# Kernel optimization log

Hardware: AMD Instinct MI355X
Metric: run time of the kernel (lower is better)

Reference implementation:

```python
import jax, jax.numpy as jnp
import numpy as np

B, D, H, R, OUT = 16384, 1024, 4, 1024, 10
LN_EPS = 1e-5


def setup_inputs() -> dict:
    key = jax.random.key(0)
    ks = jax.random.split(key, 20)
    s_in = 1.0 / np.sqrt(D)
    s_hid = 1.0 / np.sqrt(H * R)
    inp = {
        'x': jax.random.normal(ks[0], (B, D), dtype=jnp.float32),
        # block 1
        'wr1': jax.random.normal(ks[1], (H, R, D), dtype=jnp.float32) * s_in,
        'br1': jnp.zeros((H, R), dtype=jnp.float32),
        'wl1': jax.random.normal(ks[2], (H, R, D), dtype=jnp.float32) * s_in,
        'bl1': jnp.zeros((H, R), dtype=jnp.float32),
        'we1': jax.random.normal(ks[3], (D, H * R), dtype=jnp.float32) * s_hid,
        'be1': jnp.zeros((D,), dtype=jnp.float32),
        'g1': jnp.ones((D,), dtype=jnp.float32),
        'b1': jnp.zeros((D,), dtype=jnp.float32),
        # block 2
        'wr2': jax.random.normal(ks[4], (H, R, D), dtype=jnp.float32) * s_in,
        'br2': jnp.zeros((H, R), dtype=jnp.float32),
        'wl2': jax.random.normal(ks[5], (H, R, D), dtype=jnp.float32) * s_in,
        'bl2': jnp.zeros((H, R), dtype=jnp.float32),
        'we2': jax.random.normal(ks[6], (D, H * R), dtype=jnp.float32) * s_hid,
        'be2': jnp.zeros((D,), dtype=jnp.float32),
        'g2': jnp.ones((D,), dtype=jnp.float32),
        'b2': jnp.zeros((D,), dtype=jnp.float32),
        # final linear
        'wf': jax.random.normal(ks[7], (OUT, D), dtype=jnp.float32) * s_in,
        'bf': jnp.zeros((OUT,), dtype=jnp.float32),
    }
    return inp


def _bilinear_block(x, wr, br, wl, bl, we, be):
    # per-basis right/left projections batched into one einsum each: [B,D] x [H,R,D] -> [B,H,R]
    right = jnp.einsum('bd,hrd->bhr', x, wr) + br
    left = jnp.einsum('bd,hrd->bhr', x, wl) + bl
    # elementwise bilinear interaction, concat bases along last dim -> [B, H*R]
    inter = (right * left).reshape(x.shape[0], -1)
    return inter @ we.T + be  # [B, D_out]


def _layernorm(x, g, b):
    mu = jnp.mean(x, axis=-1, keepdims=True)
    var = jnp.mean(jnp.square(x - mu), axis=-1, keepdims=True)
    return (x - mu) * jax.lax.rsqrt(var + LN_EPS) * g + b


def reference(x, wr1, br1, wl1, bl1, we1, be1, g1, b1,
              wr2, br2, wl2, bl2, we2, be2, g2, b2, wf, bf):
    # block 1: bilinear + residual + layernorm
    h = _layernorm(x + _bilinear_block(x, wr1, br1, wl1, bl1, we1, be1), g1, b1)
    # block 2
    h = _layernorm(h + _bilinear_block(h, wr2, br2, wl2, bl2, we2, be2), g2, b2)
    # final linear head
    return h @ wf.T + bf
```

## Files before the change

kernel.cpp:

```cpp
#include <hip/hip_runtime.h>
#include <hip/hip_fp16.h>

#define DEV static __device__ __forceinline__

typedef _Float16 f16;
typedef _Float16 f16x8 __attribute__((ext_vector_type(8)));
typedef _Float16 f16x4 __attribute__((ext_vector_type(4)));
typedef float f32x4 __attribute__((ext_vector_type(4)));

constexpr int BATCH = 16384;
constexpr int D = 1024;
constexpr int HR = 4096;
constexpr int NOUT = 10;

__global__ void k_conv4(const float* __restrict__ s0, f16* __restrict__ d0, int n0,
                        const float* __restrict__ s1, f16* __restrict__ d1, int n1,
                        const float* __restrict__ s2, f16* __restrict__ d2, int n2,
                        const float* __restrict__ s3, f16* __restrict__ d3, int n3) {
    int i = blockIdx.x * blockDim.x + threadIdx.x;
    const int st = gridDim.x * blockDim.x;
    const int tot = n0 + n1 + n2 + n3;
    for (; i < tot; i += st) {
        const float* s; f16* d; int j = i;
        if (j < n0) { s = s0; d = d0; }
        else {
            j -= n0;
            if (j < n1) { s = s1; d = d1; }
            else {
                j -= n1;
                if (j < n2) { s = s2; d = d2; }
                else { j -= n2; s = s3; d = d3; }
            }
        }
        float4 v = reinterpret_cast<const float4*>(s)[j];
        f16x4 h;
        h[0] = (f16)v.x; h[1] = (f16)v.y; h[2] = (f16)v.z; h[3] = (f16)v.w;
        reinterpret_cast<f16x4*>(d)[j] = h;
    }
}

DEV void stage16(void* lds, const void* g) {
    __builtin_amdgcn_global_load_lds(
        (const __attribute__((address_space(1))) void*)g,
        (__attribute__((address_space(3))) void*)lds,
        16, 0, 0);
}

DEV int xcd_swz(int bid, int nwg) {
    const int cpx = nwg >> 3;
    return (bid & 7) * cpx + (bid >> 3);
}

#define VMCNT(n) asm volatile("s_waitcnt vmcnt(" #n ")" ::: "memory")
#define BAR()    __builtin_amdgcn_s_barrier()
#define PRIO(p)  __builtin_amdgcn_s_setprio(p)

__global__ __launch_bounds__(512, 2) void k_gemm_dual(
    const f16* __restrict__ Xh, const f16* __restrict__ Wr, const f16* __restrict__ Wl,
    const float* __restrict__ br, const float* __restrict__ bl,
    f16* __restrict__ inter, int MT)
{
    extern __shared__ __align__(16) char smem[];
    constexpr int NT = 16;
    constexpr int BUF = 65536;
    constexpr int OA = 0, OR = 32768, OL = 49152;

    const int swzb = xcd_swz(blockIdx.x, gridDim.x);
    const int mt = swzb % MT, nt = swzb / MT;
    const int m0 = mt * 256, n0 = nt * 128;
    const int tid = threadIdx.x;
    const int lane = tid & 63, wid = tid >> 6;
    const int wm = wid >> 2, wn = wid & 3;
    const int fr = lane & 15, fq = lane >> 4;
    const int xs = (fr & 7) << 4;
    const int dst = tid * 16;

    const int lr = tid >> 3;
    const int cb = ((tid & 7) << 4) ^ ((lr & 7) << 4);
    const char* pA0 = (const char*)Xh + (size_t)(m0 + lr)       * 2048 + cb;
    const char* pA1 = (const char*)Xh + (size_t)(m0 + 128 + lr) * 2048 + cb;
    const char* pA2 = (const char*)Xh + (size_t)(m0 + 64 + lr)  * 2048 + cb;
    const char* pA3 = (const char*)Xh + (size_t)(m0 + 192 + lr) * 2048 + cb;
    const char* pR0 = (const char*)Wr + (size_t)(n0 + lr)       * 2048 + cb;
    const char* pR1 = (const char*)Wr + (size_t)(n0 + 64 + lr)  * 2048 + cb;
    const char* pL0 = (const char*)Wl + (size_t)(n0 + lr)       * 2048 + cb;
    const char* pL1 = (const char*)Wl + (size_t)(n0 + 64 + lr)  * 2048 + cb;

#define D_AOFF(mi,mf,ks) (OA + ((mi)*128 + wm*64 + (mf)*16 + fr)*128 + ((((ks)*64) + fq*16) ^ xs))
#define D_ROFF(nf,ks)    (OR + (wn*32 + (nf)*16 + fr)*128 + ((((ks)*64) + fq*16) ^ xs))
#define D_LOFF(nf,ks)    (OL + (wn*32 + (nf)*16 + fr)*128 + ((((ks)*64) + fq*16) ^ xs))

    f16x8 a[4][2], bR[2][2], bL[2][2];
    f32x4 accR[8][2] = {};
    f32x4 accL[8][2] = {};

    stage16(smem + OA + dst, pA0);          stage16(smem + OA + 8192 + dst, pA1);
    stage16(smem + OR + dst, pR0);          stage16(smem + OR + 8192 + dst, pR1);
    stage16(smem + OL + dst, pL0);          stage16(smem + OL + 8192 + dst, pL1);
    stage16(smem + OA + 16384 + dst, pA2);  stage16(smem + OA + 24576 + dst, pA3);
    VMCNT(4);
    BAR();

    long ko = 128;
    for (int t = 0; t < NT; ++t) {
        char* base = smem + (t & 1) * BUF;
        char* nb   = smem + ((t & 1) ^ 1) * BUF;
        const bool pf = (t + 1) < NT;

#pragma unroll
        for (int mf = 0; mf < 4; ++mf)
#pragma unroll
            for (int ks = 0; ks < 2; ++ks)
                a[mf][ks] = *(const f16x8*)(base + D_AOFF(0, mf, ks));
#pragma unroll
        for (int nf = 0; nf < 2; ++nf)
#pragma unroll
            for (int ks = 0; ks < 2; ++ks)
                bR[nf][ks] = *(const f16x8*)(base + D_ROFF(nf, ks));
        if (pf) { stage16(nb + OA + dst, pA0 + ko); stage16(nb + OA + 8192 + dst, pA1 + ko); }
        PRIO(1);
#pragma unroll
        for (int mf = 0; mf < 4; ++mf)
#pragma unroll
            for (int nf = 0; nf < 2; ++nf)
#pragma unroll
                for (int ks = 0; ks < 2; ++ks)
                    accR[mf][nf] = __builtin_amdgcn_mfma_f32_16x16x32_f16(a[mf][ks], bR[nf][ks], accR[mf][nf], 0, 0, 0);
        PRIO(0);
        if (pf) { VMCNT(4); } else { VMCNT(2); }
        BAR();

#pragma unroll
        for (int nf = 0; nf < 2; ++nf)
#pragma unroll
            for (int ks = 0; ks < 2; ++ks)
                bL[nf][ks] = *(const f16x8*)(base + D_LOFF(nf, ks));
        if (pf) { stage16(nb + OR + dst, pR0 + ko); stage16(nb + OR + 8192 + dst, pR1 + ko); }
        PRIO(1);
#pragma unroll
        for (int mf = 0; mf < 4; ++mf)
#pragma unroll
            for (int nf = 0; nf < 2; ++nf)
#pragma unroll
                for (int ks = 0; ks < 2; ++ks)
                    accL[mf][nf] = __builtin_amdgcn_mfma_f32_16x16x32_f16(a[mf][ks], bL[nf][ks], accL[mf][nf], 0, 0, 0);
        PRIO(0);
        if (pf) { VMCNT(4); } else { VMCNT(0); }
        BAR();

#pragma unroll
        for (int mf = 0; mf < 4; ++mf)
#pragma unroll
            for (int ks = 0; ks < 2; ++ks)
                a[mf][ks] = *(const f16x8*)(base + D_AOFF(1, mf, ks));
        if (pf) { stage16(nb + OL + dst, pL0 + ko); stage16(nb + OL + 8192 + dst, pL1 + ko); }
        PRIO(1);
#pragma unroll
        for (int mf = 0; mf < 4; ++mf)
#pragma unroll
            for (int nf = 0; nf < 2; ++nf)
#pragma unroll
                for (int ks = 0; ks < 2; ++ks)
                    accR[4 + mf][nf] = __builtin_amdgcn_mfma_f32_16x16x32_f16(a[mf][ks], bR[nf][ks], accR[4 + mf][nf], 0, 0, 0);
        PRIO(0);
        BAR();

        if (pf) { stage16(nb + OA + 16384 + dst, pA2 + ko); stage16(nb + OA + 24576 + dst, pA3 + ko); }
        PRIO(1);
#pragma unroll
        for (int mf = 0; mf < 4; ++mf)
#pragma unroll
            for (int nf = 0; nf < 2; ++nf)
#pragma unroll
                for (int ks = 0; ks < 2; ++ks)
                    accL[4 + mf][nf] = __builtin_amdgcn_mfma_f32_16x16x32_f16(a[mf][ks], bL[nf][ks], accL[4 + mf][nf], 0, 0, 0);
        PRIO(0);
        if (pf) { VMCNT(4); }
        BAR();

        ko += 128;
    }

#pragma unroll
    for (int nf = 0; nf < 2; ++nf) {
        const int gc = n0 + wn * 32 + nf * 16 + fr;
        const float brv = br[gc], blv = bl[gc];
#pragma unroll
        for (int mi = 0; mi < 2; ++mi)
#pragma unroll
            for (int mf = 0; mf < 4; ++mf) {
                const int gr0 = m0 + wm * 128 + mi * 64 + mf * 16 + fq * 4;
#pragma unroll
                for (int j = 0; j < 4; ++j) {
                    const float rv = accR[mi * 4 + mf][nf][j] + brv;
                    const float lv = accL[mi * 4 + mf][nf][j] + blv;
                    inter[(size_t)(gr0 + j) * HR + gc] = (f16)(rv * lv);
                }
            }
    }
#undef D_AOFF
#undef D_ROFF
#undef D_LOFF
}

__global__ __launch_bounds__(512, 2) void k_gemm_expand(
    const f16* __restrict__ Ain, const f16* __restrict__ Wt,
    const float* __restrict__ be, f16* __restrict__ E, int MT)
{
    extern __shared__ __align__(16) char smem[];
    constexpr int NT = 64;
    constexpr int BUF = 65536;
    constexpr int OA = 0, OB = 32768;

    const int swzb = xcd_swz(blockIdx.x, gridDim.x);
    const int mt = swzb % MT, nt = swzb / MT;
    const int m0 = mt * 256, n0 = nt * 256;
    const int tid = threadIdx.x;
    const int lane = tid & 63, wid = tid >> 6;
    const int wm = wid >> 2, wn = wid & 3;
    const int fr = lane & 15, fq = lane >> 4;
    const int xs = (fr & 7) << 4;
    const int dst = tid * 16;

    const int lr = tid >> 3;
    const int cb = ((tid & 7) << 4) ^ ((lr & 7) << 4);
    const char* pA0 = (const char*)Ain + (size_t)(m0 + lr)       * 8192 + cb;
    const char* pA1 = (const char*)Ain + (size_t)(m0 + 128 + lr) * 8192 + cb;
    const char* pA2 = (const char*)Ain + (size_t)(m0 + 64 + lr)  * 8192 + cb;
    const char* pA3 = (const char*)Ain + (size_t)(m0 + 192 + lr) * 8192 + cb;
    const int r5 = lr & 31, wn2 = lr >> 5;
    const char* pB0 = (const char*)Wt + (size_t)(n0 + wn2 * 64 + r5)        * 8192 + cb;
    const char* pB1 = (const char*)Wt + (size_t)(n0 + (2 + wn2) * 64 + r5)  * 8192 + cb;
    const char* pB2 = (const char*)Wt + (size_t)(n0 + wn2 * 64 + 32 + r5)       * 8192 + cb;
    const char* pB3 = (const char*)Wt + (size_t)(n0 + (2 + wn2) * 64 + 32 + r5) * 8192 + cb;

#define E_AOFF(mi,mf,ks) (OA + ((mi)*128 + wm*64 + (mf)*16 + fr)*128 + ((((ks)*64) + fq*16) ^ xs))
#define E_BOFF(ni,nf,ks) (OB + ((ni)*128 + wn*32 + (nf)*16 + fr)*128 + ((((ks)*64) + fq*16) ^ xs))

    f16x8 a[4][2], b0[2][2], b1[2][2];
    f32x4 acc[8][4] = {};

    stage16(smem + OA + dst, pA0);          stage16(smem + OA + 8192 + dst, pA1);
    stage16(smem + OB + dst, pB0);          stage16(smem + OB + 8192 + dst, pB1);
    stage16(smem + OB + 16384 + dst, pB2);  stage16(smem + OB + 24576 + dst, pB3);
    stage16(smem + OA + 16384 + dst, pA2);  stage16(smem + OA + 24576 + dst, pA3);
    VMCNT(4);
    BAR();

    long ko = 128;
    for (int t = 0; t < NT; ++t) {
        char* base = smem + (t & 1) * BUF;
        char* nb   = smem + ((t & 1) ^ 1) * BUF;
        const bool pf = (t + 1) < NT;

#pragma unroll
        for (int mf = 0; mf < 4; ++mf)
#pragma unroll
            for (int ks = 0; ks < 2; ++ks)
                a[mf][ks] = *(const f16x8*)(base + E_AOFF(0, mf, ks));
#pragma unroll
        for (int nf = 0; nf < 2; ++nf)
#pragma unroll
            for (int ks = 0; ks < 2; ++ks)
                b0[nf][ks] = *(const f16x8*)(base + E_BOFF(0, nf, ks));
        if (pf) { stage16(nb + OA + dst, pA0 + ko); stage16(nb + OA + 8192 + dst, pA1 + ko); }
        PRIO(1);
#pragma unroll
        for (int mf = 0; mf < 4; ++mf)
#pragma unroll
            for (int nf = 0; nf < 2; ++nf)
#pragma unroll
                for (int ks = 0; ks < 2; ++ks)
                    acc[mf][nf] = __builtin_amdgcn_mfma_f32_16x16x32_f16(a[mf][ks], b0[nf][ks], acc[mf][nf], 0, 0, 0);
        PRIO(0);
        if (pf) { VMCNT(4); } else { VMCNT(2); }
        BAR();

#pragma unroll
        for (int nf = 0; nf < 2; ++nf)
#pragma unroll
            for (int ks = 0; ks < 2; ++ks)
                b1[nf][ks] = *(const f16x8*)(base + E_BOFF(1, nf, ks));
        if (pf) { stage16(nb + OB + dst, pB0 + ko); stage16(nb + OB + 8192 + dst, pB1 + ko); }
        PRIO(1);
#pragma unroll
        for (int mf = 0; mf < 4; ++mf)
#pragma unroll
            for (int nf = 0; nf < 2; ++nf)
#pragma unroll
                for (int ks = 0; ks < 2; ++ks)
                    acc[mf][2 + nf] = __builtin_amdgcn_mfma_f32_16x16x32_f16(a[mf][ks], b1[nf][ks], acc[mf][2 + nf], 0, 0, 0);
        PRIO(0);
        if (pf) { VMCNT(4); } else { VMCNT(0); }
        BAR();

#pragma unroll
        for (int mf = 0; mf < 4; ++mf)
#pragma unroll
            for (int ks = 0; ks < 2; ++ks)
                a[mf][ks] = *(const f16x8*)(base + E_AOFF(1, mf, ks));
        if (pf) { stage16(nb + OB + 16384 + dst, pB2 + ko); stage16(nb + OB + 24576 + dst, pB3 + ko); }
        PRIO(1);
#pragma unroll
        for (int mf = 0; mf < 4; ++mf)
#pragma unroll
            for (int nf = 0; nf < 2; ++nf)
#pragma unroll
                for (int ks = 0; ks < 2; ++ks)
                    acc[4 + mf][nf] = __builtin_amdgcn_mfma_f32_16x16x32_f16(a[mf][ks], b0[nf][ks], acc[4 + mf][nf], 0, 0, 0);
        PRIO(0);
        BAR();

        if (pf) { stage16(nb + OA + 16384 + dst, pA2 + ko); stage16(nb + OA + 24576 + dst, pA3 + ko); }
        PRIO(1);
#pragma unroll
        for (int mf = 0; mf < 4; ++mf)
#pragma unroll
            for (int nf = 0; nf < 2; ++nf)
#pragma unroll
                for (int ks = 0; ks < 2; ++ks)
                    acc[4 + mf][2 + nf] = __builtin_amdgcn_mfma_f32_16x16x32_f16(a[mf][ks], b1[nf][ks], acc[4 + mf][2 + nf], 0, 0, 0);
        PRIO(0);
        if (pf) { VMCNT(4); }
        BAR();

        ko += 128;
    }

#pragma unroll
    for (int ni = 0; ni < 2; ++ni)
#pragma unroll
        for (int nf = 0; nf < 2; ++nf) {
            const int gc = n0 + wn * 64 + ni * 32 + nf * 16 + fr;
            const float bev = be[gc];
#pragma unroll
            for (int mi = 0; mi < 2; ++mi)
#pragma unroll
                for (int mf = 0; mf < 4; ++mf) {
                    const int gr0 = m0 + wm * 128 + mi * 64 + mf * 16 + fq * 4;
#pragma unroll
                    for (int j = 0; j < 4; ++j)
                        E[(size_t)(gr0 + j) * D + gc] = (f16)(acc[mi * 4 + mf][ni * 2 + nf][j] + bev);
                }
        }
#undef E_AOFF
#undef E_BOFF
}

template <typename TR>
__global__ __launch_bounds__(256) void k_ln(
    const TR* __restrict__ X, const f16* __restrict__ Eb,
    const float* __restrict__ g, const float* __restrict__ bb,
    f16* __restrict__ Hh)
{
    const int wid = threadIdx.x >> 6, lane = threadIdx.x & 63;
    const int row = blockIdx.x * 4 + wid;
    const TR* xr = X + (size_t)row * D;
    const f16* er = Eb + (size_t)row * D;
    float v[16];
    float s = 0.f, sq = 0.f;
#pragma unroll
    for (int k = 0; k < 16; ++k) {
        const int c = lane + 64 * k;
        v[k] = (float)xr[c] + (float)er[c];
        s += v[k];
        sq += v[k] * v[k];
    }
#pragma unroll
    for (int off = 32; off; off >>= 1) {
        s += __shfl_down(s, off);
        sq += __shfl_down(sq, off);
    }
    s = __shfl(s, 0);
    sq = __shfl(sq, 0);
    const float mu = s * (1.0f / D);
    const float var = sq * (1.0f / D) - mu * mu;
    const float rs = rsqrtf(var + 1e-5f);
    f16* hh = Hh + (size_t)row * D;
#pragma unroll
    for (int k = 0; k < 16; ++k) {
        const int c = lane + 64 * k;
        const float o = (v[k] - mu) * rs * g[c] + bb[c];
        hh[c] = (f16)o;
    }
}

__global__ __launch_bounds__(256) void k_head(
    const f16* __restrict__ Hf, const float* __restrict__ Wf,
    const float* __restrict__ bf, float* __restrict__ outp)
{
    __shared__ float wfs[NOUT * D];
    for (int i = threadIdx.x; i < NOUT * D; i += 256) wfs[i] = Wf[i];
    __syncthreads();
    const int wid = threadIdx.x >> 6, lane = threadIdx.x & 63;
    const int row = blockIdx.x * 4 + wid;
    const f16* hr = Hf + (size_t)row * D;
    float hv[16];
#pragma unroll
    for (int k = 0; k < 16; ++k) hv[k] = (float)hr[lane + 64 * k];
#pragma unroll
    for (int j = 0; j < NOUT; ++j) {
        float p = 0.f;
#pragma unroll
        for (int k = 0; k < 16; ++k) p += hv[k] * wfs[j * D + lane + 64 * k];
#pragma unroll
        for (int off = 32; off; off >>= 1) p += __shfl_down(p, off);
        if (lane == 0) outp[(size_t)row * NOUT + j] = p + bf[j];
    }
}

extern "C" void kernel_launch(void* const* d_in, const int* in_sizes, int n_in,
                              void* d_out, int out_size, void* d_ws, size_t ws_size,
                              hipStream_t stream) {
    (void)in_sizes; (void)n_in; (void)out_size;
    const float* x   = (const float*)d_in[0];
    const float* wr1 = (const float*)d_in[1];
    const float* br1 = (const float*)d_in[2];
    const float* wl1 = (const float*)d_in[3];
    const float* bl1 = (const float*)d_in[4];
    const float* we1 = (const float*)d_in[5];
    const float* be1 = (const float*)d_in[6];
    const float* g1  = (const float*)d_in[7];
    const float* b1  = (const float*)d_in[8];
    const float* wr2 = (const float*)d_in[9];
    const float* br2 = (const float*)d_in[10];
    const float* wl2 = (const float*)d_in[11];
    const float* bl2 = (const float*)d_in[12];
    const float* we2 = (const float*)d_in[13];
    const float* be2 = (const float*)d_in[14];
    const float* g2  = (const float*)d_in[15];
    const float* b2  = (const float*)d_in[16];
    const float* wf  = (const float*)d_in[17];
    const float* bf  = (const float*)d_in[18];
    float* outp = (float*)d_out;

    constexpr size_t SZ_W16 = (size_t)HR * D * sizeof(f16);
    constexpr size_t SZ_A16 = (size_t)BATCH * D * sizeof(f16);
    constexpr int SMEM = 2 * 65536;

    hipFuncSetAttribute((const void*)k_gemm_dual,   hipFuncAttributeMaxDynamicSharedMemorySize, SMEM);
    hipFuncSetAttribute((const void*)k_gemm_expand, hipFuncAttributeMaxDynamicSharedMemorySize, SMEM);

    char* p = (char*)d_ws;
    f16* wrh = (f16*)p; p += SZ_W16;
    f16* wlh = (f16*)p; p += SZ_W16;
    f16* weh = (f16*)p; p += SZ_W16;
    f16* xh  = (f16*)p; p += SZ_A16;
    f16* h1h = (f16*)p; p += SZ_A16;
    f16* Eh  = (f16*)p; p += SZ_A16;
    f16* interh = (f16*)p;
    const size_t base = (size_t)(p - (char*)d_ws);
    const size_t avail = ws_size > base ? ws_size - base : 0;

    int CH = 2048;
    if ((size_t)16384 * HR * sizeof(f16) <= avail) CH = 16384;
    else if ((size_t)8192 * HR * sizeof(f16) <= avail) CH = 8192;
    else if ((size_t)4096 * HR * sizeof(f16) <= avail) CH = 4096;

    f16* h2h = xh;
    const int nch = BATCH / CH;
    const int MT = CH / 256;
    const int gDual = MT * (HR / 128);
    const int gExp  = MT * (D / 256);

    constexpr int NW4 = HR * D / 4;
    k_conv4<<<2048, 256, 0, stream>>>(x, xh, BATCH * D / 4,
                                      wr1, wrh, NW4, wl1, wlh, NW4, we1, weh, NW4);

    for (int c = 0; c < nch; ++c) {
        k_gemm_dual<<<gDual, 512, SMEM, stream>>>(xh + (size_t)c * CH * D, wrh, wlh, br1, bl1, interh, MT);
        k_gemm_expand<<<gExp, 512, SMEM, stream>>>(interh, weh, be1, Eh + (size_t)c * CH * D, MT);
    }
    k_ln<float><<<BATCH / 4, 256, 0, stream>>>(x, Eh, g1, b1, h1h);

    k_conv4<<<1536, 256, 0, stream>>>(wr2, wrh, NW4, wl2, wlh, NW4, we2, weh, NW4,
                                      nullptr, nullptr, 0);

    for (int c = 0; c < nch; ++c) {
        k_gemm_dual<<<gDual, 512, SMEM, stream>>>(h1h + (size_t)c * CH * D, wrh, wlh, br2, bl2, interh, MT);
        k_gemm_expand<<<gExp, 512, SMEM, stream>>>(interh, weh, be2, Eh + (size_t)c * CH * D, MT);
    }
    k_ln<f16><<<BATCH / 4, 256, 0, stream>>>(h1h, Eh, g2, b2, h2h);

    k_head<<<BATCH / 4, 256, 0, stream>>>(h2h, wf, bf, outp);
}
```

Before: 856.9 us.

## Fuse residual add into expand GEMM epilogue and remap XCD tile swizzle

```diff
diff --git a/kernel.cpp b/kernel.cpp
--- a/kernel.cpp
+++ b/kernel.cpp
@@ -46,9 +46,11 @@
         16, 0, 0);
 }
 
-DEV int xcd_swz(int bid, int nwg) {
-    const int cpx = nwg >> 3;
-    return (bid & 7) * cpx + (bid >> 3);
+DEV void xcd_map(int bid, int MT, int& mt, int& nt) {
+    const int x = bid & 7, q = bid >> 3;
+    const int mpx = MT >> 3;
+    nt = q / mpx;
+    mt = x * mpx + (q % mpx);
 }
 
 #define VMCNT(n) asm volatile("s_waitcnt vmcnt(" #n ")" ::: "memory")
@@ -65,8 +67,8 @@
     constexpr int BUF = 65536;
     constexpr int OA = 0, OR = 32768, OL = 49152;
 
-    const int swzb = xcd_swz(blockIdx.x, gridDim.x);
-    const int mt = swzb % MT, nt = swzb / MT;
+    int mt, nt;
+    xcd_map(blockIdx.x, MT, mt, nt);
     const int m0 = mt * 256, n0 = nt * 128;
     const int tid = threadIdx.x;
     const int lane = tid & 63, wid = tid >> 6;
@@ -203,17 +205,26 @@
 #undef D_LOFF
 }
 
-__global__ __launch_bounds__(512, 2) void k_gemm_expand(
+__global__ __launch_bounds__(512, 2) void k_gemm_expand_f32r(
     const f16* __restrict__ Ain, const f16* __restrict__ Wt,
-    const float* __restrict__ be, f16* __restrict__ E, int MT)
+    const float* __restrict__ be, const float* __restrict__ resid,
+    f16* __restrict__ E, int MT);
+__global__ __launch_bounds__(512, 2) void k_gemm_expand_f16r(
+    const f16* __restrict__ Ain, const f16* __restrict__ Wt,
+    const float* __restrict__ be, const f16* __restrict__ resid,
+    f16* __restrict__ E, int MT);
+
+template <typename TR>
+DEV void expand_body(const f16* Ain, const f16* Wt, const float* be,
+                     const TR* resid, f16* E, int MT)
 {
     extern __shared__ __align__(16) char smem[];
     constexpr int NT = 64;
     constexpr int BUF = 65536;
     constexpr int OA = 0, OB = 32768;
 
-    const int swzb = xcd_swz(blockIdx.x, gridDim.x);
-    const int mt = swzb % MT, nt = swzb / MT;
+    int mt, nt;
+    xcd_map(blockIdx.x, MT, mt, nt);
     const int m0 = mt * 256, n0 = nt * 256;
     const int tid = threadIdx.x;
     const int lane = tid & 63, wid = tid >> 6;
@@ -339,30 +350,40 @@
                 for (int mf = 0; mf < 4; ++mf) {
                     const int gr0 = m0 + wm * 128 + mi * 64 + mf * 16 + fq * 4;
 #pragma unroll
-                    for (int j = 0; j < 4; ++j)
-                        E[(size_t)(gr0 + j) * D + gc] = (f16)(acc[mi * 4 + mf][ni * 2 + nf][j] + bev);
+                    for (int j = 0; j < 4; ++j) {
+                        const float rv = (float)resid[(size_t)(gr0 + j) * D + gc];
+                        E[(size_t)(gr0 + j) * D + gc] = (f16)(acc[mi * 4 + mf][ni * 2 + nf][j] + bev + rv);
+                    }
                 }
         }
 #undef E_AOFF
 #undef E_BOFF
 }
 
-template <typename TR>
+__global__ __launch_bounds__(512, 2) void k_gemm_expand_f32r(
+    const f16* __restrict__ Ain, const f16* __restrict__ Wt,
+    const float* __restrict__ be, const float* __restrict__ resid,
+    f16* __restrict__ E, int MT)
+{ expand_body<float>(Ain, Wt, be, resid, E, MT); }
+
+__global__ __launch_bounds__(512, 2) void k_gemm_expand_f16r(
+    const f16* __restrict__ Ain, const f16* __restrict__ Wt,
+    const float* __restrict__ be, const f16* __restrict__ resid,
+    f16* __restrict__ E, int MT)
+{ expand_body<f16>(Ain, Wt, be, resid, E, MT); }
+
 __global__ __launch_bounds__(256) void k_ln(
-    const TR* __restrict__ X, const f16* __restrict__ Eb,
-    const float* __restrict__ g, const float* __restrict__ bb,
-    f16* __restrict__ Hh)
+    f16* __restrict__ EH, const float* __restrict__ g, const float* __restrict__ bb)
 {
     const int wid = threadIdx.x >> 6, lane = threadIdx.x & 63;
     const int row = blockIdx.x * 4 + wid;
-    const TR* xr = X + (size_t)row * D;
-    const f16* er = Eb + (size_t)row * D;
+    f16* er = EH + (size_t)row * D;
     float v[16];
     float s = 0.f, sq = 0.f;
 #pragma unroll
     for (int k = 0; k < 16; ++k) {
         const int c = lane + 64 * k;
-        v[k] = (float)xr[c] + (float)er[c];
+        v[k] = (float)er[c];
         s += v[k];
         sq += v[k] * v[k];
     }
@@ -376,12 +397,11 @@
     const float mu = s * (1.0f / D);
     const float var = sq * (1.0f / D) - mu * mu;
     const float rs = rsqrtf(var + 1e-5f);
-    f16* hh = Hh + (size_t)row * D;
 #pragma unroll
     for (int k = 0; k < 16; ++k) {
         const int c = lane + 64 * k;
         const float o = (v[k] - mu) * rs * g[c] + bb[c];
-        hh[c] = (f16)o;
+        er[c] = (f16)o;
     }
 }
 
@@ -438,16 +458,16 @@
     constexpr size_t SZ_A16 = (size_t)BATCH * D * sizeof(f16);
     constexpr int SMEM = 2 * 65536;
 
-    hipFuncSetAttribute((const void*)k_gemm_dual,   hipFuncAttributeMaxDynamicSharedMemorySize, SMEM);
-    hipFuncSetAttribute((const void*)k_gemm_expand, hipFuncAttributeMaxDynamicSharedMemorySize, SMEM);
+    hipFuncSetAttribute((const void*)k_gemm_dual,        hipFuncAttributeMaxDynamicSharedMemorySize, SMEM);
+    hipFuncSetAttribute((const void*)k_gemm_expand_f32r, hipFuncAttributeMaxDynamicSharedMemorySize, SMEM);
+    hipFuncSetAttribute((const void*)k_gemm_expand_f16r, hipFuncAttributeMaxDynamicSharedMemorySize, SMEM);
 
     char* p = (char*)d_ws;
     f16* wrh = (f16*)p; p += SZ_W16;
     f16* wlh = (f16*)p; p += SZ_W16;
     f16* weh = (f16*)p; p += SZ_W16;
     f16* xh  = (f16*)p; p += SZ_A16;
-    f16* h1h = (f16*)p; p += SZ_A16;
-    f16* Eh  = (f16*)p; p += SZ_A16;
+    f16* EH  = (f16*)p; p += SZ_A16;
     f16* interh = (f16*)p;
     const size_t base = (size_t)(p - (char*)d_ws);
     const size_t avail = ws_size > base ? ws_size - base : 0;
@@ -457,7 +477,6 @@
     else if ((size_t)8192 * HR * sizeof(f16) <= avail) CH = 8192;
     else if ((size_t)4096 * HR * sizeof(f16) <= avail) CH = 4096;
 
-    f16* h2h = xh;
     const int nch = BATCH / CH;
     const int MT = CH / 256;
     const int gDual = MT * (HR / 128);
@@ -469,18 +488,20 @@
 
     for (int c = 0; c < nch; ++c) {
         k_gemm_dual<<<gDual, 512, SMEM, stream>>>(xh + (size_t)c * CH * D, wrh, wlh, br1, bl1, interh, MT);
-        k_gemm_expand<<<gExp, 512, SMEM, stream>>>(interh, weh, be1, Eh + (size_t)c * CH * D, MT);
-    }
-    k_ln<float><<<BATCH / 4, 256, 0, stream>>>(x, Eh, g1, b1, h1h);
+        k_gemm_expand_f32r<<<gExp, 512, SMEM, stream>>>(interh, weh, be1, x + (size_t)c * CH * D,
+                                                        EH + (size_t)c * CH * D, MT);
+    }
+    k_ln<<<BATCH / 4, 256, 0, stream>>>(EH, g1, b1);
 
     k_conv4<<<1536, 256, 0, stream>>>(wr2, wrh, NW4, wl2, wlh, NW4, we2, weh, NW4,
                                       nullptr, nullptr, 0);
 
     for (int c = 0; c < nch; ++c) {
-        k_gemm_dual<<<gDual, 512, SMEM, stream>>>(h1h + (size_t)c * CH * D, wrh, wlh, br2, bl2, interh, MT);
-        k_gemm_expand<<<gExp, 512, SMEM, stream>>>(interh, weh, be2, Eh + (size_t)c * CH * D, MT);
-    }
-    k_ln<f16><<<BATCH / 4, 256, 0, stream>>>(h1h, Eh, g2, b2, h2h);
-
-    k_head<<<BATCH / 4, 256, 0, stream>>>(h2h, wf, bf, outp);
-}
+        k_gemm_dual<<<gDual, 512, SMEM, stream>>>(EH + (size_t)c * CH * D, wrh, wlh, br2, bl2, interh, MT);
+        k_gemm_expand_f16r<<<gExp, 512, SMEM, stream>>>(interh, weh, be2, EH + (size_t)c * CH * D,
+                                                        EH + (size_t)c * CH * D, MT);
+    }
+    k_ln<<<BATCH / 4, 256, 0, stream>>>(EH, g2, b2);
+
+    k_head<<<BATCH / 4, 256, 0, stream>>>(EH, wf, bf, outp);
+}
```

Result: faster. 803.6 us (-6.2%).
